# Optimization experiments

Measured on AMD Instinct MI355X. Metric: run time of the kernel, lower is better.

The kernel has to match this reference:

```python
import jax, jax.numpy as jnp
import numpy as np

N_NODES = 100000
N_EDGES = 1600000
IN_DIM = 128
OUT_DIM = 64


def setup_inputs() -> dict:
    key = jax.random.key(0)
    k1, k2, k3, k4, k5 = jax.random.split(key, 5)
    X = jax.random.normal(k1, (N_NODES, IN_DIM), dtype=jnp.float32)
    # reset_parameters: uniform(-stdv, stdv), stdv = 1/sqrt(output_dim)
    stdv = 1.0 / np.sqrt(OUT_DIM)
    weights = jax.random.uniform(k2, (IN_DIM, OUT_DIM), dtype=jnp.float32,
                                 minval=-stdv, maxval=stdv)
    attention_w = jax.random.normal(k3, (1, 1), dtype=jnp.float32)
    edge_src = jnp.sort(jax.random.randint(k4, (N_EDGES,), 0, N_NODES, dtype=jnp.int32))
    edge_dst = jax.random.randint(k5, (N_EDGES,), 0, N_NODES, dtype=jnp.int32)
    return {"X": X, "weights": weights, "attention_w": attention_w,
            "edge_src": edge_src, "edge_dst": edge_dst}


def reference(X, weights, attention_w, edge_src, edge_dst):
    # Dense projection: X_prime = X @ W  -> [N, OUT_DIM]
    X_prime = X @ weights
    # forward_ef: per-edge scalar feature = <X_prime[src], X_prime[dst]>  -> [E]
    src_feat = X_prime[edge_src]          # [E, OUT_DIM] irregular gather
    dst_feat = X_prime[edge_dst]          # [E, OUT_DIM] irregular gather
    edge_feature = jnp.einsum('ed,ed->e', src_feat, dst_feat)
    # edge_attentions = edge_feature[:, None] @ attention_w -> [n_heads=1, E]
    att = edge_feature * attention_w[0, 0]            # [E]
    # forward_AGNN: out[i] = sum_{e:(i->j)} att[e] * X_prime[j]
    msgs = att[:, None] * dst_feat                    # [E, OUT_DIM]
    out = jax.ops.segment_sum(msgs, edge_src, num_segments=X.shape[0])
    return out
```

## Files before the change

### kernel.cpp

```cpp
#include <hip/hip_runtime.h>
#include <stdint.h>

#define N_NODES 100000
#define N_EDGES 1600000
#define IN_DIM 128
#define OUT_DIM 64

typedef __bf16    bf16x8 __attribute__((ext_vector_type(8)));
typedef float     f32x4  __attribute__((ext_vector_type(4)));
typedef _Float16  h2     __attribute__((ext_vector_type(2)));

__device__ __forceinline__ uint16_t f2bf(float f) {
    uint32_t u = __float_as_uint(f);
    return (uint16_t)((u + 0x7fffu + ((u >> 16) & 1u)) >> 16);
}
__device__ __forceinline__ float hdot8(uint4 a, uint4 b, float c) {
#if __has_builtin(__builtin_amdgcn_fdot2)
    c = __builtin_amdgcn_fdot2(__builtin_bit_cast(h2, a.x), __builtin_bit_cast(h2, b.x), c, false);
    c = __builtin_amdgcn_fdot2(__builtin_bit_cast(h2, a.y), __builtin_bit_cast(h2, b.y), c, false);
    c = __builtin_amdgcn_fdot2(__builtin_bit_cast(h2, a.z), __builtin_bit_cast(h2, b.z), c, false);
    c = __builtin_amdgcn_fdot2(__builtin_bit_cast(h2, a.w), __builtin_bit_cast(h2, b.w), c, false);
#else
    const h2 qa[4] = {__builtin_bit_cast(h2,a.x),__builtin_bit_cast(h2,a.y),
                      __builtin_bit_cast(h2,a.z),__builtin_bit_cast(h2,a.w)};
    const h2 qb[4] = {__builtin_bit_cast(h2,b.x),__builtin_bit_cast(h2,b.y),
                      __builtin_bit_cast(h2,b.z),__builtin_bit_cast(h2,b.w)};
    #pragma unroll
    for (int i = 0; i < 4; ++i) {
        c = fmaf((float)qa[i][0], (float)qb[i][0], c);
        c = fmaf((float)qa[i][1], (float)qb[i][1], c);
    }
#endif
    return c;
}

__global__ __launch_bounds__(256) void prep(const int* __restrict__ src,
                                            const float* __restrict__ W,
                                            int* __restrict__ row_ptr,
                                            uint4* __restrict__ Wfrag) {
    const int b = blockIdx.x;
    if (b < N_EDGES / 256) {
        int e = b * 256 + threadIdx.x;
        int s = src[e];
        if (e == 0) {
            for (int i = 0; i <= s; ++i) row_ptr[i] = 0;
        } else {
            int sp = src[e - 1];
            for (int i = sp + 1; i <= s; ++i) row_ptr[i] = e;
        }
        if (e == N_EDGES - 1) {
            for (int i = s + 1; i <= N_NODES; ++i) row_ptr[i] = N_EDGES;
        }
    } else {
        int item = (b - N_EDGES / 256) * 256 + threadIdx.x;
        if (item < 1024) {
            int f = item >> 6, lane = item & 63;
            int ct = f >> 2, ks = f & 3;
            int col = ct * 16 + (lane & 15);
            int kb  = ks * 32 + (lane >> 4) * 8;
            uint32_t u[4];
            #pragma unroll
            for (int j = 0; j < 4; ++j) {
                uint32_t lo = f2bf(W[(kb + 2 * j)     * OUT_DIM + col]);
                uint32_t hi = f2bf(W[(kb + 2 * j + 1) * OUT_DIM + col]);
                u[j] = lo | (hi << 16);
            }
            Wfrag[f * 64 + lane] = make_uint4(u[0], u[1], u[2], u[3]);
        }
    }
}

__global__ __launch_bounds__(256) void gemm_xw(const float* __restrict__ X,
                                               const uint4* __restrict__ Wfrag,
                                               _Float16* __restrict__ XPh,
                                               int nRows) {
    const int t = threadIdx.x;
    const int lane = t & 63;

    bf16x8 bfr[16];
    #pragma unroll
    for (int f = 0; f < 16; ++f)
        bfr[f] = __builtin_bit_cast(bf16x8, Wfrag[f * 64 + lane]);

    const int rowBase = blockIdx.x * 64 + (t >> 6) * 16;
    const int r  = rowBase + (lane & 15);
    const int kb = (lane >> 4) * 8;
    const bool inb = r < nRows;

    f32x4 acc[4] = {{0,0,0,0},{0,0,0,0},{0,0,0,0},{0,0,0,0}};

    #pragma unroll
    for (int ks = 0; ks < 4; ++ks) {
        float4 x0 = make_float4(0.f,0.f,0.f,0.f), x1 = x0;
        if (inb) {
            const float* p = &X[(size_t)r * IN_DIM + ks * 32 + kb];
            x0 = *(const float4*)&p[0];
            x1 = *(const float4*)&p[4];
        }
        bf16x8 a;
        a[0]=(__bf16)x0.x; a[1]=(__bf16)x0.y; a[2]=(__bf16)x0.z; a[3]=(__bf16)x0.w;
        a[4]=(__bf16)x1.x; a[5]=(__bf16)x1.y; a[6]=(__bf16)x1.z; a[7]=(__bf16)x1.w;
        #pragma unroll
        for (int ct = 0; ct < 4; ++ct)
            acc[ct] = __builtin_amdgcn_mfma_f32_16x16x32_bf16(a, bfr[ct * 4 + ks], acc[ct], 0, 0, 0);
    }

    const int orow = rowBase + (lane >> 4) * 4;
    const int ocol = lane & 15;
    #pragma unroll
    for (int ct = 0; ct < 4; ++ct) {
        #pragma unroll
        for (int rr = 0; rr < 4; ++rr) {
            int gr = orow + rr;
            if (gr < nRows) XPh[(size_t)gr * OUT_DIM + ct * 16 + ocol] = (_Float16)acc[ct][rr];
        }
    }
}

__global__ __launch_bounds__(256, 6) void agnn_edge(const _Float16* __restrict__ XPh,
                                                    const int* __restrict__ row_ptr,
                                                    const int* __restrict__ dst,
                                                    const float* __restrict__ aw,
                                                    float* __restrict__ out) {
    const int t = threadIdx.x;
    const int lane = t & 63;
    const int node = blockIdx.x * 4 + (t >> 6);
    const int g = lane >> 3, sl = lane & 7;

    const int lo = row_ptr[node];
    const int hi = row_ptr[node + 1];

    const uint4 q = *(const uint4*)&XPh[(size_t)node * OUT_DIM + sl * 8];
    float acc[8] = {0.f,0.f,0.f,0.f,0.f,0.f,0.f,0.f};

    for (int base = lo; base < hi; base += 32) {
        int dx[4];
        #pragma unroll
        for (int c = 0; c < 4; ++c) {
            int e = base + c * 8 + g;
            dx[c] = (e < hi) ? dst[e] : -1;
        }
        uint4 xd[4];
        #pragma unroll
        for (int c = 0; c < 4; ++c) {
            xd[c] = make_uint4(0u, 0u, 0u, 0u);
            if (dx[c] >= 0)
                xd[c] = *(const uint4*)&XPh[(size_t)dx[c] * OUT_DIM + sl * 8];
        }
        #pragma unroll
        for (int c = 0; c < 4; ++c) {
            float p = hdot8(q, xd[c], 0.f);
            p += __shfl_xor(p, 1);
            p += __shfl_xor(p, 2);
            p += __shfl_xor(p, 4);
            const h2 d0 = __builtin_bit_cast(h2, xd[c].x);
            const h2 d1 = __builtin_bit_cast(h2, xd[c].y);
            const h2 d2 = __builtin_bit_cast(h2, xd[c].z);
            const h2 d3 = __builtin_bit_cast(h2, xd[c].w);
            acc[0] = fmaf(p, (float)d0[0], acc[0]);
            acc[1] = fmaf(p, (float)d0[1], acc[1]);
            acc[2] = fmaf(p, (float)d1[0], acc[2]);
            acc[3] = fmaf(p, (float)d1[1], acc[3]);
            acc[4] = fmaf(p, (float)d2[0], acc[4]);
            acc[5] = fmaf(p, (float)d2[1], acc[5]);
            acc[6] = fmaf(p, (float)d3[0], acc[6]);
            acc[7] = fmaf(p, (float)d3[1], acc[7]);
        }
    }

    #pragma unroll
    for (int m = 8; m <= 32; m <<= 1) {
        #pragma unroll
        for (int j = 0; j < 8; ++j) acc[j] += __shfl_xor(acc[j], m);
    }
    if (g == 0) {
        const float a = aw[0];
        float* o = &out[(size_t)node * OUT_DIM + sl * 8];
        *(float4*)&o[0] = make_float4(acc[0]*a, acc[1]*a, acc[2]*a, acc[3]*a);
        *(float4*)&o[4] = make_float4(acc[4]*a, acc[5]*a, acc[6]*a, acc[7]*a);
    }
}

extern "C" void kernel_launch(void* const* d_in, const int* in_sizes, int n_in,
                              void* d_out, int out_size, void* d_ws, size_t ws_size,
                              hipStream_t stream) {
    const float* X   = (const float*)d_in[0];
    const float* W   = (const float*)d_in[1];
    const float* aw  = (const float*)d_in[2];
    const int*   src = (const int*)d_in[3];
    const int*   dst = (const int*)d_in[4];
    float* out = (float*)d_out;

    _Float16* XPh     = (_Float16*)d_ws;
    int*      row_ptr = (int*)((char*)d_ws + (size_t)N_NODES * OUT_DIM * 2);
    uint4*    Wfrag   = (uint4*)((char*)d_ws + 13200016);

    prep<<<N_EDGES / 256 + 4, 256, 0, stream>>>(src, W, row_ptr, Wfrag);
    gemm_xw<<<(N_NODES + 63) / 64, 256, 0, stream>>>(X, Wfrag, XPh, N_NODES);
    agnn_edge<<<N_NODES / 4, 256, 0, stream>>>(XPh, row_ptr, dst, aw, out);
}
```

Baseline: 67.22 us.

## Map one node per 8-lane group in edge kernel with software-pipelined gather

Each 8-lane group now owns its own node instead of a whole wavefront sharing one node, so the eight groups in a wave walk their edge lists in lockstep, one edge at a time. The next edge's dst index and feature row are prefetched while the current one is processed. This removes the cross-group reduction and leaves only one store per node. It also reduces per-edge memory parallelism to one outstanding row gather per group, and wave time now depends on the largest degree among its eight nodes. Occupancy hint raised to 8 waves.

```diff
diff --git a/kernel.cpp b/kernel.cpp
--- a/kernel.cpp
+++ b/kernel.cpp
@@ -117,15 +117,16 @@
     }
 }
 
-__global__ __launch_bounds__(256, 6) void agnn_edge(const _Float16* __restrict__ XPh,
+__global__ __launch_bounds__(256, 8) void agnn_edge(const _Float16* __restrict__ XPh,
                                                     const int* __restrict__ row_ptr,
                                                     const int* __restrict__ dst,
                                                     const float* __restrict__ aw,
                                                     float* __restrict__ out) {
-    const int t = threadIdx.x;
+    const int t    = threadIdx.x;
     const int lane = t & 63;
-    const int node = blockIdx.x * 4 + (t >> 6);
-    const int g = lane >> 3, sl = lane & 7;
+    const int g    = lane >> 3;
+    const int sl   = lane & 7;
+    const int node = blockIdx.x * 32 + (t >> 6) * 8 + g;
 
     const int lo = row_ptr[node];
     const int hi = row_ptr[node + 1];
@@ -133,52 +134,43 @@
     const uint4 q = *(const uint4*)&XPh[(size_t)node * OUT_DIM + sl * 8];
     float acc[8] = {0.f,0.f,0.f,0.f,0.f,0.f,0.f,0.f};
 
-    for (int base = lo; base < hi; base += 32) {
-        int dx[4];
-        #pragma unroll
-        for (int c = 0; c < 4; ++c) {
-            int e = base + c * 8 + g;
-            dx[c] = (e < hi) ? dst[e] : -1;
-        }
-        uint4 xd[4];
-        #pragma unroll
-        for (int c = 0; c < 4; ++c) {
-            xd[c] = make_uint4(0u, 0u, 0u, 0u);
-            if (dx[c] >= 0)
-                xd[c] = *(const uint4*)&XPh[(size_t)dx[c] * OUT_DIM + sl * 8];
-        }
-        #pragma unroll
-        for (int c = 0; c < 4; ++c) {
-            float p = hdot8(q, xd[c], 0.f);
-            p += __shfl_xor(p, 1);
-            p += __shfl_xor(p, 2);
-            p += __shfl_xor(p, 4);
-            const h2 d0 = __builtin_bit_cast(h2, xd[c].x);
-            const h2 d1 = __builtin_bit_cast(h2, xd[c].y);
-            const h2 d2 = __builtin_bit_cast(h2, xd[c].z);
-            const h2 d3 = __builtin_bit_cast(h2, xd[c].w);
-            acc[0] = fmaf(p, (float)d0[0], acc[0]);
-            acc[1] = fmaf(p, (float)d0[1], acc[1]);
-            acc[2] = fmaf(p, (float)d1[0], acc[2]);
-            acc[3] = fmaf(p, (float)d1[1], acc[3]);
-            acc[4] = fmaf(p, (float)d2[0], acc[4]);
-            acc[5] = fmaf(p, (float)d2[1], acc[5]);
-            acc[6] = fmaf(p, (float)d3[0], acc[6]);
-            acc[7] = fmaf(p, (float)d3[1], acc[7]);
-        }
+    int  e   = lo;
+    bool act = e < hi;
+    int  d   = dst[act ? e : 0];
+    uint4 xd = *(const uint4*)&XPh[(size_t)d * OUT_DIM + sl * 8];
+
+    while (true) {
+        const int  en   = e + 1;
+        const bool actn = en < hi;
+        const int  dn   = dst[actn ? en : 0];
+        const uint4 xdn = *(const uint4*)&XPh[(size_t)dn * OUT_DIM + sl * 8];
+
+        float p = hdot8(q, xd, 0.f);
+        p += __shfl_xor(p, 1);
+        p += __shfl_xor(p, 2);
+        p += __shfl_xor(p, 4);
+        p = act ? p : 0.f;
+        const h2 d0 = __builtin_bit_cast(h2, xd.x);
+        const h2 d1 = __builtin_bit_cast(h2, xd.y);
+        const h2 d2 = __builtin_bit_cast(h2, xd.z);
+        const h2 d3 = __builtin_bit_cast(h2, xd.w);
+        acc[0] = fmaf(p, (float)d0[0], acc[0]);
+        acc[1] = fmaf(p, (float)d0[1], acc[1]);
+        acc[2] = fmaf(p, (float)d1[0], acc[2]);
+        acc[3] = fmaf(p, (float)d1[1], acc[3]);
+        acc[4] = fmaf(p, (float)d2[0], acc[4]);
+        acc[5] = fmaf(p, (float)d2[1], acc[5]);
+        acc[6] = fmaf(p, (float)d3[0], acc[6]);
+        acc[7] = fmaf(p, (float)d3[1], acc[7]);
+
+        e = en; act = actn; xd = xdn;
+        if (!__any(act)) break;
     }
 
-    #pragma unroll
-    for (int m = 8; m <= 32; m <<= 1) {
-        #pragma unroll
-        for (int j = 0; j < 8; ++j) acc[j] += __shfl_xor(acc[j], m);
-    }
-    if (g == 0) {
-        const float a = aw[0];
-        float* o = &out[(size_t)node * OUT_DIM + sl * 8];
-        *(float4*)&o[0] = make_float4(acc[0]*a, acc[1]*a, acc[2]*a, acc[3]*a);
-        *(float4*)&o[4] = make_float4(acc[4]*a, acc[5]*a, acc[6]*a, acc[7]*a);
-    }
+    const float a = aw[0];
+    float* o = &out[(size_t)node * OUT_DIM + sl * 8];
+    *(float4*)&o[0] = make_float4(acc[0]*a, acc[1]*a, acc[2]*a, acc[3]*a);
+    *(float4*)&o[4] = make_float4(acc[4]*a, acc[5]*a, acc[6]*a, acc[7]*a);
 }
 
 extern "C" void kernel_launch(void* const* d_in, const int* in_sizes, int n_in,
@@ -197,5 +189,5 @@
 
     prep<<<N_EDGES / 256 + 4, 256, 0, stream>>>(src, W, row_ptr, Wfrag);
     gemm_xw<<<(N_NODES + 63) / 64, 256, 0, stream>>>(X, Wfrag, XPh, N_NODES);
-    agnn_edge<<<N_NODES / 4, 256, 0, stream>>>(XPh, row_ptr, dst, aw, out);
+    agnn_edge<<<N_NODES / 32, 256, 0, stream>>>(XPh, row_ptr, dst, aw, out);
 }
```

Result: slower. 69.76 us (+3.8%).
